# Kernel optimization log

Measured on AMD Instinct MI355X. Metric: run time of the kernel, lower is better.

The kernel has to match this reference:

```python
import jax, jax.numpy as jnp
import numpy as np

B, C, T = 16, 64, 4096
K1, O1 = 3, 2
K2, O2 = 5, 2
D = O1 + O2  # total dendritic paths per channel
DEC = 128
TAU, THRESH = 5.0, 1.0
ALPHA = float(np.exp(-1.0 / TAU))


def setup_inputs() -> dict:
    key = jax.random.key(0)
    ks = jax.random.split(key, 14)

    def unif(k, shape, fan_in):  # torch conv/linear default init
        b = 1.0 / np.sqrt(fan_in)
        return jax.random.uniform(k, shape, minval=-b, maxval=b, dtype=jnp.float32)

    x = jax.random.normal(ks[0], (B, C, T), dtype=jnp.float32)
    # depthwise convs: torch weight (C*out_per, 1, k), group-major channel order
    w3 = unif(ks[1], (C * O1, 1, K1), K1)
    b3 = unif(ks[2], (C * O1,), K1)
    w5 = unif(ks[3], (C * O2, 1, K2), K2)
    b5 = unif(ks[4], (C * O2,), K2)
    # reduce: Conv1d(C*D -> C, k=1, groups=C) => weight (C, D)
    reduce_w = unif(ks[5], (C, D), D)
    reduce_b = unif(ks[6], (C,), D)
    latency_scale = jnp.asarray(5.0, dtype=jnp.float32)
    # xavier uniform on (C,C), diagonal zeroed
    xb = float(np.sqrt(6.0 / (C + C)))
    output_gates = jax.random.uniform(ks[7], (C, C), minval=-xb, maxval=xb, dtype=jnp.float32)
    output_gates = output_gates * (1.0 - jnp.eye(C, dtype=jnp.float32))
    mlp_w1 = unif(ks[8], (DEC, C), C)
    mlp_b1 = unif(ks[9], (DEC,), C)
    mlp_w2 = unif(ks[10], (C, DEC), DEC)
    mlp_b2 = unif(ks[11], (C,), DEC)
    return {"x": x, "w3": w3, "b3": b3, "w5": w5, "b5": b5,
            "reduce_w": reduce_w, "reduce_b": reduce_b,
            "latency_scale": latency_scale, "output_gates": output_gates,
            "mlp_w1": mlp_w1, "mlp_b1": mlp_b1, "mlp_w2": mlp_w2, "mlp_b2": mlp_b2}


def _dwconv(x, w, b, k):
    # depthwise grouped conv, 'same' padding, groups=C
    pad = (k - 1) // 2
    y = jax.lax.conv_general_dilated(
        x, w, window_strides=(1,), padding=[(pad, pad)],
        dimension_numbers=("NCH", "OIH", "NCH"), feature_group_count=C)
    return y + b[None, :, None]


def _forward(x, w3, b3, w5, b5, reduce_w, reduce_b,
             latency_scale, output_gates, mlp_w1, mlp_b1, mlp_w2, mlp_b2):
    # encoder: multi-path depthwise convs -> dendritic_drive (B,C,D,T)
    o3 = _dwconv(x, w3, b3, K1).reshape(B, C, O1, T)
    o5 = _dwconv(x, w5, b5, K2).reshape(B, C, O2, T)
    dendritic_drive = jnp.concatenate([o3, o5], axis=2)  # (B,C,D,T)
    # grouped 1x1 reduce: per-channel mix over D
    summed = jnp.einsum("bcdt,cd->bct", dendritic_drive, reduce_w) + reduce_b[None, :, None]

    # LIF latency: leaky integrate over T, first-crossing time (T if none)
    def step(V, d_t):
        V = ALPHA * V + (1.0 - ALPHA) * d_t
        return V, V >= THRESH

    _, spikes = jax.lax.scan(step, jnp.zeros((B, C), dtype=summed.dtype),
                             jnp.moveaxis(summed, 2, 0))  # spikes: (T,B,C) bool
    any_fired = spikes.any(axis=0)
    first_t = jnp.argmax(spikes, axis=0)  # first True index
    true_latency = jnp.where(any_fired, first_t, T).astype(summed.dtype)  # (B,C)

    scale = jnp.maximum(latency_scale, 0.001)
    act = jnp.exp(-true_latency / scale)  # (B,C)
    mixed = act @ output_gates.T
    h = jax.nn.relu(mixed @ mlp_w1.T + mlp_b1)
    raw_pred = h @ mlp_w2.T + mlp_b2
    pred_latency = jnp.clip(jax.nn.softplus(raw_pred), 0.0, float(T))
    return pred_latency, true_latency, act, dendritic_drive


def reference(x, w3, b3, w5, b5, reduce_w, reduce_b,
              latency_scale, output_gates, mlp_w1, mlp_b1, mlp_w2, mlp_b2):
    return _forward(x, w3, b3, w5, b5, reduce_w, reduce_b,
                    latency_scale, output_gates, mlp_w1, mlp_b1, mlp_w2, mlp_b2)
```

## Files before the change

kernel.cpp:

```cpp
#include <hip/hip_runtime.h>
#include <math.h>

#define NB 16
#define NC 64
#define NT 4096
#define NDEC 128

#define ALPHA_F 0.81873075307798185867f
#define ONEMA_F 0.18126924692201814133f
#define Q16_F   0.040762203978366216f

__global__ __launch_bounds__(256) void conv_lif_kernel(
    const float* __restrict__ x,
    const float* __restrict__ w3, const float* __restrict__ b3,
    const float* __restrict__ w5, const float* __restrict__ b5,
    const float* __restrict__ rw, const float* __restrict__ rb,
    float* __restrict__ out)
{
    __shared__ __align__(16) float s_x[4 + NT + 4];
    __shared__ float s_sum[NT + 256];
    __shared__ float s_scan[256];
    __shared__ int   s_wmin[4];

    const int bc  = blockIdx.x;
    const int c   = bc & (NC - 1);
    const int tid = threadIdx.x;

    if (tid < 4) { s_x[tid] = 0.f; s_x[4 + NT + tid] = 0.f; }
    {
        const float4* x4  = (const float4*)(x + (size_t)bc * NT);
        float4*       sx4 = (float4*)(s_x + 4);
        #pragma unroll
        for (int i = 0; i < 4; ++i) sx4[i * 256 + tid] = x4[i * 256 + tid];
    }

    const float w30a = w3[(c*2+0)*3+0], w30b = w3[(c*2+0)*3+1], w30c = w3[(c*2+0)*3+2];
    const float w31a = w3[(c*2+1)*3+0], w31b = w3[(c*2+1)*3+1], w31c = w3[(c*2+1)*3+2];
    const float b30 = b3[c*2+0], b31 = b3[c*2+1];
    const float* w50p = w5 + (c*2+0)*5;
    const float* w51p = w5 + (c*2+1)*5;
    const float w50a=w50p[0], w50b=w50p[1], w50c=w50p[2], w50d=w50p[3], w50e=w50p[4];
    const float w51a=w51p[0], w51b=w51p[1], w51c=w51p[2], w51d=w51p[3], w51e=w51p[4];
    const float b50 = b5[c*2+0], b51 = b5[c*2+1];
    const float rw0 = rw[c*4+0], rw1 = rw[c*4+1], rw2 = rw[c*4+2], rw3 = rw[c*4+3];
    const float rbc = rb[c];

    __syncthreads();

    float* dd = out + 3072 + (size_t)bc * (4 * NT);
    #pragma unroll 4
    for (int i = 0; i < 16; ++i) {
        int t = i * 256 + tid;
        float xm2 = s_x[t + 2];
        float xm1 = s_x[t + 3];
        float x0  = s_x[t + 4];
        float xp1 = s_x[t + 5];
        float xp2 = s_x[t + 6];
        float o30 = fmaf(w30c, xp1, fmaf(w30b, x0, fmaf(w30a, xm1, b30)));
        float o31 = fmaf(w31c, xp1, fmaf(w31b, x0, fmaf(w31a, xm1, b31)));
        float o50 = fmaf(w50e, xp2, fmaf(w50d, xp1, fmaf(w50c, x0,
                    fmaf(w50b, xm1, fmaf(w50a, xm2, b50)))));
        float o51 = fmaf(w51e, xp2, fmaf(w51d, xp1, fmaf(w51c, x0,
                    fmaf(w51b, xm1, fmaf(w51a, xm2, b51)))));
        dd[t]          = o30;
        dd[NT + t]     = o31;
        dd[2 * NT + t] = o50;
        dd[3 * NT + t] = o51;
        s_sum[t + (t >> 4)] = fmaf(rw3, o51, fmaf(rw2, o50,
                              fmaf(rw1, o31, fmaf(rw0, o30, rbc))));
    }
    __syncthreads();

    const int t0 = tid * 16;
    float dv[16];
    #pragma unroll
    for (int j = 0; j < 16; ++j) dv[j] = s_sum[t0 + tid + j];

    float V = 0.f;
    #pragma unroll
    for (int j = 0; j < 16; ++j)
        V = __fadd_rn(__fmul_rn(ALPHA_F, V), __fmul_rn(ONEMA_F, dv[j]));
    s_scan[tid] = V;
    __syncthreads();

    float coef = Q16_F;
    for (int off = 1; off < 256; off <<= 1) {
        float prev = (tid >= off) ? s_scan[tid - off] : 0.f;
        __syncthreads();
        s_scan[tid] = fmaf(coef, prev, s_scan[tid]);
        __syncthreads();
        coef *= coef;
    }

    float Vin = (tid == 0) ? 0.f : s_scan[tid - 1];
    V = Vin;
    int firstt = NT;
    #pragma unroll
    for (int j = 0; j < 16; ++j) {
        V = __fadd_rn(__fmul_rn(ALPHA_F, V), __fmul_rn(ONEMA_F, dv[j]));
        if (V >= 1.0f && firstt == NT) firstt = t0 + j;
    }

    int m = firstt;
    #pragma unroll
    for (int off = 32; off > 0; off >>= 1) m = min(m, __shfl_down(m, off));
    if ((tid & 63) == 0) s_wmin[tid >> 6] = m;
    __syncthreads();
    if (tid == 0) {
        int r = min(min(s_wmin[0], s_wmin[1]), min(s_wmin[2], s_wmin[3]));
        out[1024 + bc] = (float)r;
    }
}

__global__ __launch_bounds__(128) void head_kernel(
    const float* __restrict__ lat_scale,
    const float* __restrict__ og,
    const float* __restrict__ w1, const float* __restrict__ b1,
    const float* __restrict__ w2, const float* __restrict__ b2,
    float* __restrict__ out)
{
    __shared__ float act_s[NC];
    __shared__ float mixed_s[NC];
    __shared__ float h_s[NDEC];
    const int b   = blockIdx.x;
    const int tid = threadIdx.x;
    const float scale = fmaxf(lat_scale[0], 0.001f);

    if (tid < NC) {
        float tl = out[1024 + b * NC + tid];
        float a  = expf(-tl / scale);
        act_s[tid] = a;
        out[2048 + b * NC + tid] = a;
    }
    __syncthreads();

    if (tid < NC) {
        float mx = 0.f;
        #pragma unroll 8
        for (int cc = 0; cc < NC; ++cc) mx = fmaf(act_s[cc], og[tid * NC + cc], mx);
        mixed_s[tid] = mx;
    }
    __syncthreads();

    {
        float h = b1[tid];
        #pragma unroll 8
        for (int i = 0; i < NC; ++i) h = fmaf(mixed_s[i], w1[tid * NC + i], h);
        h_s[tid] = fmaxf(h, 0.f);
    }
    __syncthreads();

    if (tid < NC) {
        float r = b2[tid];
        #pragma unroll 8
        for (int j = 0; j < NDEC; ++j) r = fmaf(h_s[j], w2[tid * NDEC + j], r);
        float sp = fmaxf(r, 0.f) + log1pf(expf(-fabsf(r)));
        out[b * NC + tid] = fminf(sp, (float)NT);
    }
}

extern "C" void kernel_launch(void* const* d_in, const int* in_sizes, int n_in,
                              void* d_out, int out_size, void* d_ws, size_t ws_size,
                              hipStream_t stream) {
    const float* x  = (const float*)d_in[0];
    const float* w3 = (const float*)d_in[1];
    const float* b3 = (const float*)d_in[2];
    const float* w5 = (const float*)d_in[3];
    const float* b5 = (const float*)d_in[4];
    const float* rw = (const float*)d_in[5];
    const float* rb = (const float*)d_in[6];
    const float* ls = (const float*)d_in[7];
    const float* og = (const float*)d_in[8];
    const float* w1 = (const float*)d_in[9];
    const float* b1 = (const float*)d_in[10];
    const float* w2 = (const float*)d_in[11];
    const float* b2 = (const float*)d_in[12];
    float* out = (float*)d_out;

    conv_lif_kernel<<<NB * NC, 256, 0, stream>>>(x, w3, b3, w5, b5, rw, rb, out);
    head_kernel<<<NB, 128, 0, stream>>>(ls, og, w1, b1, w2, b2, out);
}
```

Measured before the change: 115.7 us.

## Fuse head MLP into conv/LIF kernel via last-block atomic counter

Merges the separate head kernel into the conv/LIF kernel. Each block increments a global counter, and the last block to finish computes act, mixing, the MLP and softplus for all 16 batches. Conv outputs are now written with nontemporal stores. This removes one kernel launch and its gap but adds a memset launch and serializes the head onto a single block. The head then runs over all batches with 256 threads instead of 16 blocks of 128.

```diff
diff --git a/kernel.cpp b/kernel.cpp
--- a/kernel.cpp
+++ b/kernel.cpp
@@ -10,17 +10,23 @@
 #define ONEMA_F 0.18126924692201814133f
 #define Q16_F   0.040762203978366216f
 
-__global__ __launch_bounds__(256) void conv_lif_kernel(
+__global__ __launch_bounds__(256) void conv_lif_fused(
     const float* __restrict__ x,
     const float* __restrict__ w3, const float* __restrict__ b3,
     const float* __restrict__ w5, const float* __restrict__ b5,
     const float* __restrict__ rw, const float* __restrict__ rb,
-    float* __restrict__ out)
+    const float* __restrict__ lat_scale,
+    const float* __restrict__ og,
+    const float* __restrict__ w1, const float* __restrict__ b1,
+    const float* __restrict__ w2, const float* __restrict__ b2,
+    float* __restrict__ out, int* __restrict__ counter)
 {
-    __shared__ __align__(16) float s_x[4 + NT + 4];
-    __shared__ float s_sum[NT + 256];
-    __shared__ float s_scan[256];
-    __shared__ int   s_wmin[4];
+    __shared__ __align__(16) float smem[4104 + 4352 + 256 + 4];
+    __shared__ int s_is_last;
+    float* s_x    = smem;
+    float* s_sum  = smem + 4104;
+    float* s_scan = smem + 8456;
+    int*   s_wmin = (int*)(smem + 8712);
 
     const int bc  = blockIdx.x;
     const int c   = bc & (NC - 1);
@@ -62,10 +68,10 @@
                     fmaf(w50b, xm1, fmaf(w50a, xm2, b50)))));
         float o51 = fmaf(w51e, xp2, fmaf(w51d, xp1, fmaf(w51c, x0,
                     fmaf(w51b, xm1, fmaf(w51a, xm2, b51)))));
-        dd[t]          = o30;
-        dd[NT + t]     = o31;
-        dd[2 * NT + t] = o50;
-        dd[3 * NT + t] = o51;
+        __builtin_nontemporal_store(o30, dd + t);
+        __builtin_nontemporal_store(o31, dd + NT + t);
+        __builtin_nontemporal_store(o50, dd + 2 * NT + t);
+        __builtin_nontemporal_store(o51, dd + 3 * NT + t);
         s_sum[t + (t >> 4)] = fmaf(rw3, o51, fmaf(rw2, o50,
                               fmaf(rw1, o31, fmaf(rw0, o30, rbc))));
     }
@@ -92,8 +98,7 @@
         coef *= coef;
     }
 
-    float Vin = (tid == 0) ? 0.f : s_scan[tid - 1];
-    V = Vin;
+    V = (tid == 0) ? 0.f : s_scan[tid - 1];
     int firstt = NT;
     #pragma unroll
     for (int j = 0; j < 16; ++j) {
@@ -109,53 +114,63 @@
     if (tid == 0) {
         int r = min(min(s_wmin[0], s_wmin[1]), min(s_wmin[2], s_wmin[3]));
         out[1024 + bc] = (float)r;
+        __threadfence();
+        int prev = atomicAdd(counter, 1);
+        s_is_last = (prev == (int)gridDim.x - 1);
     }
-}
+    __syncthreads();
+    if (!s_is_last) return;
 
-__global__ __launch_bounds__(128) void head_kernel(
-    const float* __restrict__ lat_scale,
-    const float* __restrict__ og,
-    const float* __restrict__ w1, const float* __restrict__ b1,
-    const float* __restrict__ w2, const float* __restrict__ b2,
-    float* __restrict__ out)
-{
-    __shared__ float act_s[NC];
-    __shared__ float mixed_s[NC];
-    __shared__ float h_s[NDEC];
-    const int b   = blockIdx.x;
-    const int tid = threadIdx.x;
+    __threadfence();
+    float* s_act   = smem;
+    float* s_mixed = smem + 1024;
+    float* s_h     = smem + 2048;
+
     const float scale = fmaxf(lat_scale[0], 0.001f);
 
-    if (tid < NC) {
-        float tl = out[1024 + b * NC + tid];
+    #pragma unroll
+    for (int k = tid; k < 1024; k += 256) {
+        float tl = out[1024 + k];
         float a  = expf(-tl / scale);
-        act_s[tid] = a;
-        out[2048 + b * NC + tid] = a;
+        s_act[k] = a;
+        out[2048 + k] = a;
     }
     __syncthreads();
 
-    if (tid < NC) {
+    #pragma unroll
+    for (int k = tid; k < 1024; k += 256) {
+        int b = k >> 6, cc0 = k & 63;
+        const float* ob = og + cc0 * NC;
+        const float* ab = s_act + b * NC;
         float mx = 0.f;
         #pragma unroll 8
-        for (int cc = 0; cc < NC; ++cc) mx = fmaf(act_s[cc], og[tid * NC + cc], mx);
-        mixed_s[tid] = mx;
+        for (int cc = 0; cc < NC; ++cc) mx = fmaf(ab[cc], ob[cc], mx);
+        s_mixed[k] = mx;
     }
     __syncthreads();
 
-    {
-        float h = b1[tid];
+    #pragma unroll
+    for (int k = tid; k < 2048; k += 256) {
+        int b = k >> 7, j = k & 127;
+        const float* mb = s_mixed + b * NC;
+        const float* wj = w1 + j * NC;
+        float h = b1[j];
         #pragma unroll 8
-        for (int i = 0; i < NC; ++i) h = fmaf(mixed_s[i], w1[tid * NC + i], h);
-        h_s[tid] = fmaxf(h, 0.f);
+        for (int i = 0; i < NC; ++i) h = fmaf(mb[i], wj[i], h);
+        s_h[k] = fmaxf(h, 0.f);
     }
     __syncthreads();
 
-    if (tid < NC) {
-        float r = b2[tid];
+    #pragma unroll
+    for (int k = tid; k < 1024; k += 256) {
+        int b = k >> 6, cc0 = k & 63;
+        const float* hb = s_h + b * NDEC;
+        const float* wc = w2 + cc0 * NDEC;
+        float r = b2[cc0];
         #pragma unroll 8
-        for (int j = 0; j < NDEC; ++j) r = fmaf(h_s[j], w2[tid * NDEC + j], r);
+        for (int j = 0; j < NDEC; ++j) r = fmaf(hb[j], wc[j], r);
         float sp = fmaxf(r, 0.f) + log1pf(expf(-fabsf(r)));
-        out[b * NC + tid] = fminf(sp, (float)NT);
+        out[k] = fminf(sp, (float)NT);
     }
 }
 
@@ -176,7 +191,9 @@
     const float* w2 = (const float*)d_in[11];
     const float* b2 = (const float*)d_in[12];
     float* out = (float*)d_out;
+    int* counter = (int*)d_ws;
 
-    conv_lif_kernel<<<NB * NC, 256, 0, stream>>>(x, w3, b3, w5, b5, rw, rb, out);
-    head_kernel<<<NB, 128, 0, stream>>>(ls, og, w1, b1, w2, b2, out);
+    hipMemsetAsync(counter, 0, sizeof(int), stream);
+    conv_lif_fused<<<NB * NC, 256, 0, stream>>>(
+        x, w3, b3, w5, b5, rw, rb, ls, og, w1, b1, w2, b2, out, counter);
 }
```

New measurement: 181.1 us. +56.5%, slower.
